# Kernel tuning notes

Measured on AMD Instinct MI355X. Metric: run time of the kernel, lower is better.

Reference implementation:

```python
import jax, jax.numpy as jnp
import numpy as np

V = 20000      # nodes
L = 4          # topological levels
PER = 5000     # nodes per level
DEG = 16       # parents per node
D = 512        # d_model
H = 8          # nheads
Cd = D // H    # head_dim
E = (L - 1) * PER * DEG


def setup_inputs() -> dict:
    rng = np.random.default_rng(0)
    node_levels = np.repeat(np.arange(L), PER).astype(np.int64)
    srcs, tgts = [], []
    for l in range(1, L):
        srcs.append(rng.integers((l - 1) * PER, l * PER, size=PER * DEG))
        tgts.append(np.repeat(np.arange(l * PER, (l + 1) * PER), DEG))
    edge_index = np.stack([np.concatenate(srcs), np.concatenate(tgts)]).astype(np.int64)
    key = jax.random.key(0)
    ks = jax.random.split(key, 14)
    glorot = 0.05
    def p(k, shape):
        return jax.random.normal(k, shape, jnp.float32) * glorot
    return {
        'node_feats': jax.random.normal(ks[0], (V, D), jnp.float32),
        'edge_feats': jax.random.normal(ks[1], (E, D), jnp.float32),
        'edge_index': jnp.asarray(edge_index),
        'node_levels': jnp.asarray(node_levels),
        'n_levels': L,
        'Wn_bu': p(ks[2], (D, D)), 'We_bu': p(ks[3], (D, D)), 'attn_bu': p(ks[4], (H, 3 * Cd)),
        'Wo_bu': p(ks[5], (D, D)), 'bo_bu': jnp.zeros((D,), jnp.float32),
        'Wn_td': p(ks[6], (D, D)), 'We_td': p(ks[7], (D, D)), 'attn_td': p(ks[8], (H, 3 * Cd)),
        'Wo_td': p(ks[9], (D, D)), 'bo_td': jnp.zeros((D,), jnp.float32),
    }


def _direction(node_feats, edge_feats, Wn, We, attn_w, Wo, bo, src, tgt, node_lv, n_levels):
    Vn = node_feats.shape[0]
    scale = (3 * Cd) ** -0.5
    aw_j, aw_i, aw_e = attn_w[:, :Cd], attn_w[:, Cd:2 * Cd], attn_w[:, 2 * Cd:]
    # edge features are static across levels -> project once
    ep = (edge_feats @ We).reshape(-1, H, Cd)            # E h c
    ep_alpha = jnp.einsum('ehc,hc->eh', ep, aw_e)        # E h
    edge_lv = node_lv[tgt]                               # level of each edge's target
    for l in range(1, n_levels):
        xp = (node_feats @ Wn).reshape(Vn, H, Cd)        # V h c
        aj = jnp.einsum('vhc,hc->vh', xp, aw_j)
        ai = jnp.einsum('vhc,hc->vh', xp, aw_i)
        a = (aj[src] + ai[tgt] + ep_alpha) * scale       # E h
        a = jnp.where((edge_lv == l)[:, None], a, -jnp.inf)
        # self-loop: edge feature filled with 0.0 -> only x_j/x_i terms
        sa = (aj + ai) * scale                           # V h
        m = jnp.maximum(jax.ops.segment_max(a, tgt, num_segments=Vn), sa)
        we = jnp.exp(a - m[tgt])                         # E h (0 for masked edges)
        ws = jnp.exp(sa - m)                             # V h
        denom = jax.ops.segment_sum(we, tgt, num_segments=Vn) + ws
        agg = jax.ops.segment_sum(we[:, :, None] * xp[src], tgt, num_segments=Vn) + ws[:, :, None] * xp
        out = (agg / denom[:, :, None]).reshape(Vn, H * Cd) @ Wo + bo  # to_out (dropout=eval identity)
        node_feats = jnp.where((node_lv == l)[:, None], out, node_feats)
    return node_feats


def reference(node_feats, edge_feats, edge_index, node_levels, n_levels,
              Wn_bu, We_bu, attn_bu, Wo_bu, bo_bu,
              Wn_td, We_td, attn_td, Wo_td, bo_td):
    src, tgt = edge_index[0], edge_index[1]
    # bottom-up: edges as given, topo levels 0..L-1
    bu = _direction(node_feats, edge_feats, Wn_bu, We_bu, attn_bu, Wo_bu, bo_bu,
                    src, tgt, node_levels, n_levels)
    # top-down: reversed edges, topo levels reversed
    lv_td = (n_levels - 1) - node_levels
    td = _direction(node_feats, edge_feats, Wn_td, We_td, attn_td, Wo_td, bo_td,
                    tgt, src, lv_td, n_levels)
    return jnp.stack([td, bu], axis=0)  # (topdown, bottomup)
```

## Files before the change

kernel.cpp:

```cpp
#include <hip/hip_runtime.h>

#define NV 20000
#define NE 240000
#define PER 5000
#define DEG 16
#define EPB 80000
#define SCALE 0.07216878364870323f
#define MAXDEG 96

typedef __attribute__((ext_vector_type(8))) short s16x8;
typedef __attribute__((ext_vector_type(4))) float f32x4;

__device__ inline ushort bf16rne(float x) {
    uint32_t u = __float_as_uint(x);
    u += 0x7fffu + ((u >> 16) & 1u);
    return (ushort)(u >> 16);
}
__device__ inline s16x8 cvt8(float4 a, float4 b) {
    s16x8 v;
    v[0] = (short)bf16rne(a.x); v[1] = (short)bf16rne(a.y);
    v[2] = (short)bf16rne(a.z); v[3] = (short)bf16rne(a.w);
    v[4] = (short)bf16rne(b.x); v[5] = (short)bf16rne(b.y);
    v[6] = (short)bf16rne(b.z); v[7] = (short)bf16rne(b.w);
    return v;
}

__global__ void init_copy(const float* __restrict__ nf, float* __restrict__ out) {
    int i = blockIdx.x * 256 + threadIdx.x;
    float4 v = reinterpret_cast<const float4*>(nf)[i];
    reinterpret_cast<float4*>(out)[i] = v;
    reinterpret_cast<float4*>(out + (size_t)NV * 512)[i] = v;
}

__global__ void fold_kernel(
    const float* __restrict__ Wn_bu, const float* __restrict__ attn_bu,
    const float* __restrict__ Wn_td, const float* __restrict__ attn_td,
    const float* __restrict__ We_bu, const float* __restrict__ We_td,
    ushort* __restrict__ foldT)
{
    int idx = blockIdx.x * 256 + threadIdx.x;
    if (idx >= 3 * 8192) return;
    int arr = idx >> 13;
    int r = idx & 8191;
    int d = r >> 4;
    int o = r & 15;
    int h = o & 7;
    const float* W; const float* attn; int awOff;
    if (arr == 0)      { W = Wn_bu; attn = attn_bu; awOff = (o < 8) ? 0 : 64; }
    else if (arr == 1) { W = Wn_td; attn = attn_td; awOff = (o < 8) ? 0 : 64; }
    else               { W = (o < 8) ? We_bu : We_td; attn = (o < 8) ? attn_bu : attn_td; awOff = 128; }
    float s = 0.f;
    for (int cc = 0; cc < 64; ++cc)
        s += W[d * 512 + h * 64 + cc] * attn[h * 192 + awOff + cc];
    foldT[arr * 8192 + o * 512 + d] = bf16rne(s);
}

__global__ __launch_bounds__(256) void prep_w(
    const float* __restrict__ W0, const float* __restrict__ W1,
    const float* __restrict__ W2, const float* __restrict__ W3,
    ushort* __restrict__ Bt)
{
    __shared__ float T[64][65];
    const int t = threadIdx.x;
    const int b = blockIdx.x;
    const int mat = b >> 6;
    const int tk = (b >> 3) & 7, tn = b & 7;
    const float* W = (mat == 0) ? W0 : (mat == 1) ? W1 : (mat == 2) ? W2 : W3;
    const int k0 = tk * 64, n0 = tn * 64;
    #pragma unroll
    for (int i = 0; i < 4; ++i) {
        int r = (t >> 4) * 4 + i;
        int c = (t & 15) * 4;
        float4 v = *reinterpret_cast<const float4*>(W + (size_t)(k0 + r) * 512 + n0 + c);
        T[r][c + 0] = v.x; T[r][c + 1] = v.y; T[r][c + 2] = v.z; T[r][c + 3] = v.w;
    }
    __syncthreads();
    #pragma unroll
    for (int i = 0; i < 4; ++i) {
        int n = (t >> 4) * 4 + i;
        int c = (t & 15) * 4;
        ushort4 o;
        o.x = bf16rne(T[c + 0][n]); o.y = bf16rne(T[c + 1][n]);
        o.z = bf16rne(T[c + 2][n]); o.w = bf16rne(T[c + 3][n]);
        *reinterpret_cast<ushort4*>(Bt + (size_t)mat * 262144 + (size_t)(n0 + n) * 512 + k0 + c) = o;
    }
}

__global__ __launch_bounds__(256) void rowdot_mfma(
    const float* __restrict__ A, int nTiles,
    const ushort* __restrict__ Bt16, float* __restrict__ out)
{
    __shared__ ushort Bs[16][520];
    const int t = threadIdx.x;
    for (int i = t; i < 16 * 512; i += 256)
        Bs[i >> 9][i & 511] = Bt16[i];
    __syncthreads();
    const int wave = t >> 6, lane = t & 63;
    const int tile = blockIdx.x * 4 + wave;
    if (tile >= nTiles) return;
    const int fr = lane & 15;
    const int fk = (lane >> 4) * 8;
    const float* Ar = A + (size_t)tile * 16 * 512 + (size_t)fr * 512;
    f32x4 acc = {0.f, 0.f, 0.f, 0.f};
    #pragma unroll
    for (int k0 = 0; k0 < 512; k0 += 32) {
        float4 a0 = *reinterpret_cast<const float4*>(Ar + k0 + fk);
        float4 a1 = *reinterpret_cast<const float4*>(Ar + k0 + fk + 4);
        s16x8 av = cvt8(a0, a1);
        s16x8 bv = *reinterpret_cast<const s16x8*>(&Bs[fr][k0 + fk]);
        acc = __builtin_amdgcn_mfma_f32_16x16x32_bf16(av, bv, acc, 0, 0, 0);
    }
    #pragma unroll
    for (int i = 0; i < 4; ++i) {
        int r = tile * 16 + (lane >> 4) * 4 + i;
        out[(size_t)r * 16 + (lane & 15)] = acc[i];
    }
}

__global__ __launch_bounds__(256) void gemm_mfma(
    const float* __restrict__ A, const ushort* __restrict__ Bt,
    float* __restrict__ C, int M, const float* __restrict__ bias)
{
    __shared__ ushort As[64][40];
    __shared__ ushort Bs[64][40];
    const int t = threadIdx.x;
    const int wave = t >> 6, lane = t & 63;
    const int row0 = blockIdx.x * 64, col0 = blockIdx.y * 64;
    const int wm = (wave >> 1) * 32, wn = (wave & 1) * 32;
    const int sm = t >> 2;
    const int sk = (t & 3) * 8;
    const int fr = lane & 15;
    const int fk = (lane >> 4) * 8;
    const bool aok = (row0 + sm) < M;
    const float* Ap = A + (size_t)(row0 + sm) * 512;
    const ushort* Bp = Bt + (size_t)(col0 + sm) * 512;
    f32x4 acc[2][2];
    #pragma unroll
    for (int mi = 0; mi < 2; ++mi)
        #pragma unroll
        for (int ni = 0; ni < 2; ++ni) acc[mi][ni] = (f32x4){0.f, 0.f, 0.f, 0.f};

    for (int k0 = 0; k0 < 512; k0 += 32) {
        float4 a0, a1;
        if (aok) {
            a0 = *reinterpret_cast<const float4*>(Ap + k0 + sk);
            a1 = *reinterpret_cast<const float4*>(Ap + k0 + sk + 4);
        } else {
            a0 = make_float4(0.f, 0.f, 0.f, 0.f);
            a1 = a0;
        }
        *reinterpret_cast<s16x8*>(&As[sm][sk]) = cvt8(a0, a1);
        *reinterpret_cast<s16x8*>(&Bs[sm][sk]) =
            *reinterpret_cast<const s16x8*>(Bp + k0 + sk);
        __syncthreads();
        s16x8 af[2], bf[2];
        af[0] = *reinterpret_cast<const s16x8*>(&As[wm + fr][fk]);
        af[1] = *reinterpret_cast<const s16x8*>(&As[wm + 16 + fr][fk]);
        bf[0] = *reinterpret_cast<const s16x8*>(&Bs[wn + fr][fk]);
        bf[1] = *reinterpret_cast<const s16x8*>(&Bs[wn + 16 + fr][fk]);
        acc[0][0] = __builtin_amdgcn_mfma_f32_16x16x32_bf16(af[0], bf[0], acc[0][0], 0, 0, 0);
        acc[0][1] = __builtin_amdgcn_mfma_f32_16x16x32_bf16(af[0], bf[1], acc[0][1], 0, 0, 0);
        acc[1][0] = __builtin_amdgcn_mfma_f32_16x16x32_bf16(af[1], bf[0], acc[1][0], 0, 0, 0);
        acc[1][1] = __builtin_amdgcn_mfma_f32_16x16x32_bf16(af[1], bf[1], acc[1][1], 0, 0, 0);
        __syncthreads();
    }
    #pragma unroll
    for (int mi = 0; mi < 2; ++mi) {
        #pragma unroll
        for (int ni = 0; ni < 2; ++ni) {
            int c = col0 + wn + ni * 16 + (lane & 15);
            float bb = bias ? bias[c] : 0.f;
            #pragma unroll
            for (int i = 0; i < 4; ++i) {
                int r = row0 + wm + mi * 16 + (lane >> 4) * 4 + i;
                if (r < M) C[(size_t)r * 512 + c] = acc[mi][ni][i] + bb;
            }
        }
    }
}

__global__ void csr_zero(int* cnt) {
    int i = blockIdx.x * 256 + threadIdx.x;
    if (i < 15000) cnt[i] = 0;
}
__global__ void csr_count(const int* __restrict__ ei, int* __restrict__ cnt) {
    int e = blockIdx.x * 256 + threadIdx.x;
    if (e >= NE) return;
    int lv = e / EPB;
    int local = ei[e] - lv * PER;
    atomicAdd(&cnt[lv * PER + local], 1);
}
__global__ void csr_scan(const int* __restrict__ cnt, int* __restrict__ rptr) {
    __shared__ int part[256];
    int lv = blockIdx.x, t = threadIdx.x;
    int s = 0;
    if (t < 250)
        for (int j = 0; j < 20; ++j) s += cnt[lv * PER + t * 20 + j];
    part[t] = s;
    __syncthreads();
    if (t == 0) {
        int run = 0;
        for (int i = 0; i < 250; ++i) { int v = part[i]; part[i] = run; run += v; }
        rptr[lv * 5001 + 5000] = run;
    }
    __syncthreads();
    if (t < 250) {
        int run = part[t];
        for (int j = 0; j < 20; ++j) {
            int idx = t * 20 + j;
            rptr[lv * 5001 + idx] = run;
            run += cnt[lv * PER + idx];
        }
    }
}
__global__ void csr_offinit(const int* __restrict__ rptr, int* __restrict__ off) {
    int i = blockIdx.x * 256 + threadIdx.x;
    if (i >= 15000) return;
    int lv = i / PER, local = i - lv * PER;
    off[i] = rptr[lv * 5001 + local];
}
__global__ void csr_fill(const int* __restrict__ ei, int* __restrict__ off, int* __restrict__ eids) {
    int e = blockIdx.x * 256 + threadIdx.x;
    if (e >= NE) return;
    int lv = e / EPB;
    int local = ei[e] - lv * PER;
    int pos = atomicAdd(&off[lv * PER + local], 1);
    eids[lv * EPB + pos] = e;
}

template<bool FIXED>
__global__ __launch_bounds__(512) void attn_kernel(
    const float* __restrict__ xp,
    const float* __restrict__ ajai,
    const float* __restrict__ epA,
    const int* __restrict__ srcArr,
    const int* __restrict__ rptr,
    const int* __restrict__ eids,
    int eBase,
    int base,
    int tgtLocOff,
    int dirOff,
    float* __restrict__ aggn)
{
    __shared__ float Lwe[MAXDEG][8];
    __shared__ int   Lsrci[MAXDEG];
    __shared__ float Lws[8];
    __shared__ float Ldenom[8];
    const int t = blockIdx.x;
    const int tid = threadIdx.x;
    const int tgtXp = tgtLocOff + t;

    int deg, ebase;
    if (FIXED) { deg = DEG; ebase = eBase + t * DEG; }
    else       { int r0 = rptr[t]; deg = rptr[t + 1] - r0; ebase = r0; }
    if (deg > MAXDEG) deg = MAXDEG;

    for (int kk = tid; kk < deg * 8; kk += 512) {
        int k = kk >> 3, h = kk & 7;
        int e = FIXED ? (ebase + k) : eids[ebase + k];
        int src = srcArr[e] - base;
        float lg = (ajai[src * 16 + h] + ajai[tgtXp * 16 + 8 + h] + epA[(size_t)e * 16 + dirOff + h]) * SCALE;
        Lwe[k][h] = lg;
        if (h == 0) Lsrci[k] = src;
    }
    if (tid < 8) Lws[tid] = (ajai[tgtXp * 16 + tid] + ajai[tgtXp * 16 + 8 + tid]) * SCALE;
    __syncthreads();
    if (tid < 8) {
        float m = Lws[tid];
        for (int k = 0; k < deg; ++k) m = fmaxf(m, Lwe[k][tid]);
        float dsum = 0.f;
        for (int k = 0; k < deg; ++k) {
            float w = expf(Lwe[k][tid] - m);
            Lwe[k][tid] = w;
            dsum += w;
        }
        float wsv = expf(Lws[tid] - m);
        Lws[tid] = wsv;
        Ldenom[tid] = dsum + wsv;
    }
    __syncthreads();
    const int h = tid >> 6, c = tid & 63;
    float acc = Lws[h] * xp[(size_t)tgtXp * 512 + h * 64 + c];
    if (FIXED) {
        #pragma unroll
        for (int k = 0; k < DEG; ++k)
            acc += Lwe[k][h] * xp[(size_t)Lsrci[k] * 512 + h * 64 + c];
    } else {
        #pragma unroll 4
        for (int k = 0; k < deg; ++k)
            acc += Lwe[k][h] * xp[(size_t)Lsrci[k] * 512 + h * 64 + c];
    }
    aggn[(size_t)t * 512 + h * 64 + c] = acc / Ldenom[h];
}

extern "C" void kernel_launch(void* const* d_in, const int* in_sizes, int n_in,
                              void* d_out, int out_size, void* d_ws, size_t ws_size,
                              hipStream_t stream) {
    const float* node_feats = (const float*)d_in[0];
    const float* edge_feats = (const float*)d_in[1];
    const int*   edge_index = (const int*)d_in[2];
    const float* Wn_bu  = (const float*)d_in[5];
    const float* We_bu  = (const float*)d_in[6];
    const float* attn_bu = (const float*)d_in[7];
    const float* Wo_bu  = (const float*)d_in[8];
    const float* bo_bu  = (const float*)d_in[9];
    const float* Wn_td  = (const float*)d_in[10];
    const float* We_td  = (const float*)d_in[11];
    const float* attn_td = (const float*)d_in[12];
    const float* Wo_td  = (const float*)d_in[13];
    const float* bo_td  = (const float*)d_in[14];

    float* out = (float*)d_out;
    float* td = out;
    float* bu = out + (size_t)NV * 512;

    float* ws   = (float*)d_ws;
    float* xp   = ws;
    float* aggn = xp + 5120000;
    float* ajai = aggn + 2560000;
    float* epA  = ajai + 160000;
    int* cnt  = (int*)(epA + 3840000);
    int* off  = cnt + 15000;
    int* rptr = off + 15000;
    int* eids = rptr + 15008;
    ushort* BtW   = (ushort*)(eids + 240000);
    ushort* foldT = BtW + 4 * 262144;

    const int* ei_src = edge_index;
    const int* ei_tgt = edge_index + NE;

    init_copy<<<10000, 256, 0, stream>>>(node_feats, out);
    fold_kernel<<<96, 256, 0, stream>>>(Wn_bu, attn_bu, Wn_td, attn_td, We_bu, We_td, foldT);
    prep_w<<<256, 256, 0, stream>>>(Wn_bu, Wo_bu, Wn_td, Wo_td, BtW);
    rowdot_mfma<<<3750, 256, 0, stream>>>(edge_feats, 15000, foldT + 2 * 8192, epA);

    csr_zero<<<59, 256, 0, stream>>>(cnt);
    csr_count<<<938, 256, 0, stream>>>(ei_src, cnt);
    csr_scan<<<3, 256, 0, stream>>>(cnt, rptr);
    csr_offinit<<<59, 256, 0, stream>>>(rptr, off);
    csr_fill<<<938, 256, 0, stream>>>(ei_src, off, eids);

    for (int l = 1; l <= 3; ++l) {
        int base = (l - 1) * PER;
        gemm_mfma<<<dim3(157, 8), 256, 0, stream>>>(bu + (size_t)base * 512, BtW, xp, 10000, nullptr);
        rowdot_mfma<<<157, 256, 0, stream>>>(bu + (size_t)base * 512, 625, foldT, ajai);
        attn_kernel<true><<<5000, 512, 0, stream>>>(xp, ajai, epA, ei_src,
                                                    nullptr, nullptr, (l - 1) * EPB,
                                                    base, PER, 0, aggn);
        gemm_mfma<<<dim3(79, 8), 256, 0, stream>>>(aggn, BtW + 262144, bu + (size_t)(l * PER) * 512, 5000, bo_bu);
    }
    for (int ltd = 1; ltd <= 3; ++ltd) {
        int lvIdx = 3 - ltd;
        int base = lvIdx * PER;
        gemm_mfma<<<dim3(157, 8), 256, 0, stream>>>(td + (size_t)base * 512, BtW + 2 * 262144, xp, 10000, nullptr);
        rowdot_mfma<<<157, 256, 0, stream>>>(td + (size_t)base * 512, 625, foldT + 8192, ajai);
        attn_kernel<false><<<5000, 512, 0, stream>>>(xp, ajai, epA, ei_tgt,
                                                     rptr + lvIdx * 5001, eids + lvIdx * EPB, 0,
                                                     base, 0, 8, aggn);
        gemm_mfma<<<dim3(79, 8), 256, 0, stream>>>(aggn, BtW + 3 * 262144, td + (size_t)base * 512, 5000, bo_td);
    }
}
```

Measured before the change: 1.248 ms.

## Batch bottom-up and top-down directions per level and fold attention dots into GEMM

The bottom-up and top-down passes now run together at each level: each GEMM and the attention kernel cover both directions in one launch, selected by grid z or block index. The attention-logit projections (aj/ai) become extra output columns of the node projection GEMM (Bt padded to 576 columns), which removes the separate rowdot launches. The attention kernel handles four targets per block with float4 loads, and the CSR offset init is merged into the scan. Launch count drops and each grid is larger, at the cost of duplicated workspace buffers and some wasted zero-padded GEMM columns.

```diff
diff --git a/kernel.cpp b/kernel.cpp
--- a/kernel.cpp
+++ b/kernel.cpp
@@ -36,29 +36,47 @@
     const float* __restrict__ Wn_bu, const float* __restrict__ attn_bu,
     const float* __restrict__ Wn_td, const float* __restrict__ attn_td,
     const float* __restrict__ We_bu, const float* __restrict__ We_td,
-    ushort* __restrict__ foldT)
+    ushort* __restrict__ Bt1_bu, ushort* __restrict__ Bt1_td,
+    ushort* __restrict__ foldE)
 {
     int idx = blockIdx.x * 256 + threadIdx.x;
-    if (idx >= 3 * 8192) return;
-    int arr = idx >> 13;
-    int r = idx & 8191;
-    int d = r >> 4;
-    int o = r & 15;
-    int h = o & 7;
-    const float* W; const float* attn; int awOff;
-    if (arr == 0)      { W = Wn_bu; attn = attn_bu; awOff = (o < 8) ? 0 : 64; }
-    else if (arr == 1) { W = Wn_td; attn = attn_td; awOff = (o < 8) ? 0 : 64; }
-    else               { W = (o < 8) ? We_bu : We_td; attn = (o < 8) ? attn_bu : attn_td; awOff = 128; }
-    float s = 0.f;
-    for (int cc = 0; cc < 64; ++cc)
-        s += W[d * 512 + h * 64 + cc] * attn[h * 192 + awOff + cc];
-    foldT[arr * 8192 + o * 512 + d] = bf16rne(s);
+    const int SZ = 64 * 512;
+    if (idx < 2 * SZ) {
+        int arr = idx / SZ;
+        int r = idx - arr * SZ;
+        int o = r >> 9;
+        int d = r & 511;
+        ushort val = 0;
+        if (o < 16) {
+            const float* W    = arr ? Wn_td   : Wn_bu;
+            const float* attn = arr ? attn_td : attn_bu;
+            int h = o & 7;
+            int awOff = (o < 8) ? 0 : 64;
+            float s = 0.f;
+            for (int cc = 0; cc < 64; ++cc)
+                s += W[d * 512 + h * 64 + cc] * attn[h * 192 + awOff + cc];
+            val = bf16rne(s);
+        }
+        (arr ? Bt1_td : Bt1_bu)[(size_t)(512 + o) * 512 + d] = val;
+    } else if (idx < 2 * SZ + 16 * 512) {
+        int r = idx - 2 * SZ;
+        int o = r >> 9;
+        int d = r & 511;
+        const float* W    = (o < 8) ? We_bu   : We_td;
+        const float* attn = (o < 8) ? attn_bu : attn_td;
+        int h = o & 7;
+        float s = 0.f;
+        for (int cc = 0; cc < 64; ++cc)
+            s += W[d * 512 + h * 64 + cc] * attn[h * 192 + 128 + cc];
+        foldE[o * 512 + d] = bf16rne(s);
+    }
 }
 
 __global__ __launch_bounds__(256) void prep_w(
     const float* __restrict__ W0, const float* __restrict__ W1,
     const float* __restrict__ W2, const float* __restrict__ W3,
-    ushort* __restrict__ Bt)
+    ushort* __restrict__ Bt1_bu, ushort* __restrict__ Bt2_bu,
+    ushort* __restrict__ Bt1_td, ushort* __restrict__ Bt2_td)
 {
     __shared__ float T[64][65];
     const int t = threadIdx.x;
@@ -66,6 +84,7 @@
     const int mat = b >> 6;
     const int tk = (b >> 3) & 7, tn = b & 7;
     const float* W = (mat == 0) ? W0 : (mat == 1) ? W1 : (mat == 2) ? W2 : W3;
+    ushort* outp = (mat == 0) ? Bt1_bu : (mat == 1) ? Bt2_bu : (mat == 2) ? Bt1_td : Bt2_td;
     const int k0 = tk * 64, n0 = tn * 64;
     #pragma unroll
     for (int i = 0; i < 4; ++i) {
@@ -82,7 +101,7 @@
         ushort4 o;
         o.x = bf16rne(T[c + 0][n]); o.y = bf16rne(T[c + 1][n]);
         o.z = bf16rne(T[c + 2][n]); o.w = bf16rne(T[c + 3][n]);
-        *reinterpret_cast<ushort4*>(Bt + (size_t)mat * 262144 + (size_t)(n0 + n) * 512 + k0 + c) = o;
+        *reinterpret_cast<ushort4*>(outp + (size_t)(n0 + n) * 512 + k0 + c) = o;
     }
 }
 
@@ -117,12 +136,20 @@
     }
 }
 
-__global__ __launch_bounds__(256) void gemm_mfma(
-    const float* __restrict__ A, const ushort* __restrict__ Bt,
-    float* __restrict__ C, int M, const float* __restrict__ bias)
+__global__ __launch_bounds__(256) void gemm1_fused(
+    const float* __restrict__ Abu, const float* __restrict__ Atd,
+    const ushort* __restrict__ Btbu, const ushort* __restrict__ Bttd,
+    float* __restrict__ xpbu, float* __restrict__ xptd,
+    float* __restrict__ ajbu, float* __restrict__ ajtd)
 {
     __shared__ ushort As[64][40];
     __shared__ ushort Bs[64][40];
+    const int z = blockIdx.z;
+    const float* A   = z ? Atd  : Abu;
+    const ushort* Bt = z ? Bttd : Btbu;
+    float* xp = z ? xptd : xpbu;
+    float* aj = z ? ajtd : ajbu;
+    const int M = 10000;
     const int t = threadIdx.x;
     const int wave = t >> 6, lane = t & 63;
     const int row0 = blockIdx.x * 64, col0 = blockIdx.y * 64;
@@ -169,7 +196,79 @@
         #pragma unroll
         for (int ni = 0; ni < 2; ++ni) {
             int c = col0 + wn + ni * 16 + (lane & 15);
-            float bb = bias ? bias[c] : 0.f;
+            #pragma unroll
+            for (int i = 0; i < 4; ++i) {
+                int r = row0 + wm + mi * 16 + (lane >> 4) * 4 + i;
+                if (r < M) {
+                    if (c < 512)       xp[(size_t)r * 512 + c] = acc[mi][ni][i];
+                    else if (c < 528)  aj[(size_t)r * 16 + (c - 512)] = acc[mi][ni][i];
+                }
+            }
+        }
+    }
+}
+
+__global__ __launch_bounds__(256) void gemm2_fused(
+    const float* __restrict__ Abu, const float* __restrict__ Atd,
+    const ushort* __restrict__ Btbu, const ushort* __restrict__ Bttd,
+    float* __restrict__ Cbu, float* __restrict__ Ctd,
+    const float* __restrict__ bbu, const float* __restrict__ btd)
+{
+    __shared__ ushort As[64][40];
+    __shared__ ushort Bs[64][40];
+    const int z = blockIdx.z;
+    const float* A   = z ? Atd  : Abu;
+    const ushort* Bt = z ? Bttd : Btbu;
+    float* C = z ? Ctd : Cbu;
+    const float* bias = z ? btd : bbu;
+    const int M = 5000;
+    const int t = threadIdx.x;
+    const int wave = t >> 6, lane = t & 63;
+    const int row0 = blockIdx.x * 64, col0 = blockIdx.y * 64;
+    const int wm = (wave >> 1) * 32, wn = (wave & 1) * 32;
+    const int sm = t >> 2;
+    const int sk = (t & 3) * 8;
+    const int fr = lane & 15;
+    const int fk = (lane >> 4) * 8;
+    const bool aok = (row0 + sm) < M;
+    const float* Ap = A + (size_t)(row0 + sm) * 512;
+    const ushort* Bp = Bt + (size_t)(col0 + sm) * 512;
+    f32x4 acc[2][2];
+    #pragma unroll
+    for (int mi = 0; mi < 2; ++mi)
+        #pragma unroll
+        for (int ni = 0; ni < 2; ++ni) acc[mi][ni] = (f32x4){0.f, 0.f, 0.f, 0.f};
+
+    for (int k0 = 0; k0 < 512; k0 += 32) {
+        float4 a0, a1;
+        if (aok) {
+            a0 = *reinterpret_cast<const float4*>(Ap + k0 + sk);
+            a1 = *reinterpret_cast<const float4*>(Ap + k0 + sk + 4);
+        } else {
+            a0 = make_float4(0.f, 0.f, 0.f, 0.f);
+            a1 = a0;
+        }
+        *reinterpret_cast<s16x8*>(&As[sm][sk]) = cvt8(a0, a1);
+        *reinterpret_cast<s16x8*>(&Bs[sm][sk]) =
+            *reinterpret_cast<const s16x8*>(Bp + k0 + sk);
+        __syncthreads();
+        s16x8 af[2], bf[2];
+        af[0] = *reinterpret_cast<const s16x8*>(&As[wm + fr][fk]);
+        af[1] = *reinterpret_cast<const s16x8*>(&As[wm + 16 + fr][fk]);
+        bf[0] = *reinterpret_cast<const s16x8*>(&Bs[wn + fr][fk]);
+        bf[1] = *reinterpret_cast<const s16x8*>(&Bs[wn + 16 + fr][fk]);
+        acc[0][0] = __builtin_amdgcn_mfma_f32_16x16x32_bf16(af[0], bf[0], acc[0][0], 0, 0, 0);
+        acc[0][1] = __builtin_amdgcn_mfma_f32_16x16x32_bf16(af[0], bf[1], acc[0][1], 0, 0, 0);
+        acc[1][0] = __builtin_amdgcn_mfma_f32_16x16x32_bf16(af[1], bf[0], acc[1][0], 0, 0, 0);
+        acc[1][1] = __builtin_amdgcn_mfma_f32_16x16x32_bf16(af[1], bf[1], acc[1][1], 0, 0, 0);
+        __syncthreads();
+    }
+    #pragma unroll
+    for (int mi = 0; mi < 2; ++mi) {
+        #pragma unroll
+        for (int ni = 0; ni < 2; ++ni) {
+            int c = col0 + wn + ni * 16 + (lane & 15);
+            float bb = bias[c];
             #pragma unroll
             for (int i = 0; i < 4; ++i) {
                 int r = row0 + wm + mi * 16 + (lane >> 4) * 4 + i;
@@ -190,7 +289,8 @@
     int local = ei[e] - lv * PER;
     atomicAdd(&cnt[lv * PER + local], 1);
 }
-__global__ void csr_scan(const int* __restrict__ cnt, int* __restrict__ rptr) {
+__global__ void csr_scan(const int* __restrict__ cnt, int* __restrict__ rptr,
+                         int* __restrict__ off) {
     __shared__ int part[256];
     int lv = blockIdx.x, t = threadIdx.x;
     int s = 0;
@@ -209,15 +309,10 @@
         for (int j = 0; j < 20; ++j) {
             int idx = t * 20 + j;
             rptr[lv * 5001 + idx] = run;
+            off[lv * PER + idx] = run;
             run += cnt[lv * PER + idx];
         }
     }
-}
-__global__ void csr_offinit(const int* __restrict__ rptr, int* __restrict__ off) {
-    int i = blockIdx.x * 256 + threadIdx.x;
-    if (i >= 15000) return;
-    int lv = i / PER, local = i - lv * PER;
-    off[i] = rptr[lv * 5001 + local];
 }
 __global__ void csr_fill(const int* __restrict__ ei, int* __restrict__ off, int* __restrict__ eids) {
     int e = blockIdx.x * 256 + threadIdx.x;
@@ -228,69 +323,86 @@
     eids[lv * EPB + pos] = e;
 }
 
-template<bool FIXED>
-__global__ __launch_bounds__(512) void attn_kernel(
-    const float* __restrict__ xp,
-    const float* __restrict__ ajai,
+__global__ __launch_bounds__(512) void attn_fused(
+    const float* __restrict__ xp_bu, const float* __restrict__ ajai_bu,
+    const float* __restrict__ xp_td, const float* __restrict__ ajai_td,
     const float* __restrict__ epA,
-    const int* __restrict__ srcArr,
+    const int* __restrict__ ei_src, const int* __restrict__ ei_tgt,
     const int* __restrict__ rptr,
     const int* __restrict__ eids,
-    int eBase,
-    int base,
-    int tgtLocOff,
-    int dirOff,
-    float* __restrict__ aggn)
-{
-    __shared__ float Lwe[MAXDEG][8];
-    __shared__ int   Lsrci[MAXDEG];
-    __shared__ float Lws[8];
-    __shared__ float Ldenom[8];
-    const int t = blockIdx.x;
+    int eBaseBU, int baseBU, int baseTD,
+    float* __restrict__ aggn_bu, float* __restrict__ aggn_td)
+{
+    __shared__ float Lwe[4][MAXDEG][8];
+    __shared__ int   Lsrci[4][MAXDEG];
+    __shared__ float Lws[4][8];
+    __shared__ float Ldenom[4][8];
     const int tid = threadIdx.x;
-    const int tgtXp = tgtLocOff + t;
+    const int q = tid >> 7, f = tid & 127;
+    const bool isBU = blockIdx.x < 1250;
+    const int t = (isBU ? blockIdx.x : blockIdx.x - 1250) * 4 + q;
+
+    const float* xp   = isBU ? xp_bu   : xp_td;
+    const float* ajai = isBU ? ajai_bu : ajai_td;
+    const int* srcArr = isBU ? ei_src  : ei_tgt;
+    const int base    = isBU ? baseBU  : baseTD;
+    const int tgtXp   = (isBU ? 5000 : 0) + t;
+    const int dirOff  = isBU ? 0 : 8;
+    float* aggn       = isBU ? aggn_bu : aggn_td;
 
     int deg, ebase;
-    if (FIXED) { deg = DEG; ebase = eBase + t * DEG; }
-    else       { int r0 = rptr[t]; deg = rptr[t + 1] - r0; ebase = r0; }
+    if (isBU) { deg = DEG; ebase = eBaseBU + t * DEG; }
+    else      { int r0 = rptr[t]; deg = rptr[t + 1] - r0; ebase = r0; }
     if (deg > MAXDEG) deg = MAXDEG;
 
-    for (int kk = tid; kk < deg * 8; kk += 512) {
+    const float tAi = ajai[tgtXp * 16 + 8 + (f & 7)];
+    for (int kk = f; kk < deg * 8; kk += 128) {
         int k = kk >> 3, h = kk & 7;
-        int e = FIXED ? (ebase + k) : eids[ebase + k];
+        int e = isBU ? (ebase + k) : eids[ebase + k];
         int src = srcArr[e] - base;
-        float lg = (ajai[src * 16 + h] + ajai[tgtXp * 16 + 8 + h] + epA[(size_t)e * 16 + dirOff + h]) * SCALE;
-        Lwe[k][h] = lg;
-        if (h == 0) Lsrci[k] = src;
-    }
-    if (tid < 8) Lws[tid] = (ajai[tgtXp * 16 + tid] + ajai[tgtXp * 16 + 8 + tid]) * SCALE;
-    __syncthreads();
-    if (tid < 8) {
-        float m = Lws[tid];
-        for (int k = 0; k < deg; ++k) m = fmaxf(m, Lwe[k][tid]);
+        float lg = (ajai[src * 16 + h] + tAi + epA[(size_t)e * 16 + dirOff + h]) * SCALE;
+        Lwe[q][k][h] = lg;
+        if (h == 0) Lsrci[q][k] = src;
+    }
+    if (f < 8) Lws[q][f] = (ajai[tgtXp * 16 + f] + ajai[tgtXp * 16 + 8 + f]) * SCALE;
+    __syncthreads();
+    if (f < 8) {
+        float m = Lws[q][f];
+        for (int k = 0; k < deg; ++k) m = fmaxf(m, Lwe[q][k][f]);
         float dsum = 0.f;
         for (int k = 0; k < deg; ++k) {
-            float w = expf(Lwe[k][tid] - m);
-            Lwe[k][tid] = w;
+            float w = expf(Lwe[q][k][f] - m);
+            Lwe[q][k][f] = w;
             dsum += w;
         }
-        float wsv = expf(Lws[tid] - m);
-        Lws[tid] = wsv;
-        Ldenom[tid] = dsum + wsv;
-    }
-    __syncthreads();
-    const int h = tid >> 6, c = tid & 63;
-    float acc = Lws[h] * xp[(size_t)tgtXp * 512 + h * 64 + c];
-    if (FIXED) {
+        float wsv = expf(Lws[q][f] - m);
+        Lws[q][f] = wsv;
+        Ldenom[q][f] = dsum + wsv;
+    }
+    __syncthreads();
+    const int h = f >> 4;
+    const float4* xp4 = reinterpret_cast<const float4*>(xp);
+    float4 xv = xp4[(size_t)tgtXp * 128 + f];
+    float w0 = Lws[q][h];
+    float ax = w0 * xv.x, ay = w0 * xv.y, az = w0 * xv.z, aw = w0 * xv.w;
+    if (isBU) {
         #pragma unroll
-        for (int k = 0; k < DEG; ++k)
-            acc += Lwe[k][h] * xp[(size_t)Lsrci[k] * 512 + h * 64 + c];
+        for (int k = 0; k < DEG; ++k) {
+            float w = Lwe[q][k][h];
+            float4 v = xp4[(size_t)Lsrci[q][k] * 128 + f];
+            ax += w * v.x; ay += w * v.y; az += w * v.z; aw += w * v.w;
+        }
     } else {
         #pragma unroll 4
-        for (int k = 0; k < deg; ++k)
-            acc += Lwe[k][h] * xp[(size_t)Lsrci[k] * 512 + h * 64 + c];
-    }
-    aggn[(size_t)t * 512 + h * 64 + c] = acc / Ldenom[h];
+        for (int k = 0; k < deg; ++k) {
+            float w = Lwe[q][k][h];
+            float4 v = xp4[(size_t)Lsrci[q][k] * 128 + f];
+            ax += w * v.x; ay += w * v.y; az += w * v.z; aw += w * v.w;
+        }
+    }
+    float inv = 1.f / Ldenom[q][h];
+    float4 r; r.x = ax * inv; r.y = ay * inv; r.z = az * inv; r.w = aw * inv;
+    reinterpret_cast<float4*>(aggn)[(size_t)t * 128 + f] = r;
 }
 
 extern "C" void kernel_launch(void* const* d_in, const int* in_sizes, int n_in,
@@ -314,49 +426,53 @@
     float* td = out;
     float* bu = out + (size_t)NV * 512;
 
-    float* ws   = (float*)d_ws;
-    float* xp   = ws;
-    float* aggn = xp + 5120000;
-    float* ajai = aggn + 2560000;
-    float* epA  = ajai + 160000;
+    float* ws      = (float*)d_ws;
+    float* xp_bu   = ws;
+    float* xp_td   = xp_bu + 5120000;
+    float* aggn_bu = xp_td + 5120000;
+    float* aggn_td = aggn_bu + 2560000;
+    float* ajai_bu = aggn_td + 2560000;
+    float* ajai_td = ajai_bu + 160000;
+    float* epA     = ajai_td + 160000;
     int* cnt  = (int*)(epA + 3840000);
     int* off  = cnt + 15000;
     int* rptr = off + 15000;
     int* eids = rptr + 15008;
-    ushort* BtW   = (ushort*)(eids + 240000);
-    ushort* foldT = BtW + 4 * 262144;
+    ushort* Bt1_bu = (ushort*)(eids + 240000);
+    ushort* Bt1_td = Bt1_bu + 294912;
+    ushort* Bt2_bu = Bt1_td + 294912;
+    ushort* Bt2_td = Bt2_bu + 262144;
+    ushort* foldE  = Bt2_td + 262144;
 
     const int* ei_src = edge_index;
     const int* ei_tgt = edge_index + NE;
 
     init_copy<<<10000, 256, 0, stream>>>(node_feats, out);
-    fold_kernel<<<96, 256, 0, stream>>>(Wn_bu, attn_bu, Wn_td, attn_td, We_bu, We_td, foldT);
-    prep_w<<<256, 256, 0, stream>>>(Wn_bu, Wo_bu, Wn_td, Wo_td, BtW);
-    rowdot_mfma<<<3750, 256, 0, stream>>>(edge_feats, 15000, foldT + 2 * 8192, epA);
+    fold_kernel<<<288, 256, 0, stream>>>(Wn_bu, attn_bu, Wn_td, attn_td, We_bu, We_td,
+                                         Bt1_bu, Bt1_td, foldE);
+    prep_w<<<256, 256, 0, stream>>>(Wn_bu, Wo_bu, Wn_td, Wo_td,
+                                    Bt1_bu, Bt2_bu, Bt1_td, Bt2_td);
+    rowdot_mfma<<<3750, 256, 0, stream>>>(edge_feats, 15000, foldE, epA);
 
     csr_zero<<<59, 256, 0, stream>>>(cnt);
     csr_count<<<938, 256, 0, stream>>>(ei_src, cnt);
-    csr_scan<<<3, 256, 0, stream>>>(cnt, rptr);
-    csr_offinit<<<59, 256, 0, stream>>>(rptr, off);
+    csr_scan<<<3, 256, 0, stream>>>(cnt, rptr, off);
     csr_fill<<<938, 256, 0, stream>>>(ei_src, off, eids);
 
-    for (int l = 1; l <= 3; ++l) {
-        int base = (l - 1) * PER;
-        gemm_mfma<<<dim3(157, 8), 256, 0, stream>>>(bu + (size_t)base * 512, BtW, xp, 10000, nullptr);
-        rowdot_mfma<<<157, 256, 0, stream>>>(bu + (size_t)base * 512, 625, foldT, ajai);
-        attn_kernel<true><<<5000, 512, 0, stream>>>(xp, ajai, epA, ei_src,
-                                                    nullptr, nullptr, (l - 1) * EPB,
-                                                    base, PER, 0, aggn);
-        gemm_mfma<<<dim3(79, 8), 256, 0, stream>>>(aggn, BtW + 262144, bu + (size_t)(l * PER) * 512, 5000, bo_bu);
-    }
-    for (int ltd = 1; ltd <= 3; ++ltd) {
-        int lvIdx = 3 - ltd;
-        int base = lvIdx * PER;
-        gemm_mfma<<<dim3(157, 8), 256, 0, stream>>>(td + (size_t)base * 512, BtW + 2 * 262144, xp, 10000, nullptr);
-        rowdot_mfma<<<157, 256, 0, stream>>>(td + (size_t)base * 512, 625, foldT + 8192, ajai);
-        attn_kernel<false><<<5000, 512, 0, stream>>>(xp, ajai, epA, ei_tgt,
-                                                     rptr + lvIdx * 5001, eids + lvIdx * EPB, 0,
-                                                     base, 0, 8, aggn);
-        gemm_mfma<<<dim3(79, 8), 256, 0, stream>>>(aggn, BtW + 3 * 262144, td + (size_t)base * 512, 5000, bo_td);
-    }
-}
+    for (int i = 1; i <= 3; ++i) {
+        const int l = i, lvIdx = 3 - i;
+        const int baseBU = (l - 1) * PER;
+        const int baseTD = lvIdx * PER;
+        gemm1_fused<<<dim3(157, 9, 2), 256, 0, stream>>>(
+            bu + (size_t)baseBU * 512, td + (size_t)baseTD * 512,
+            Bt1_bu, Bt1_td, xp_bu, xp_td, ajai_bu, ajai_td);
+        attn_fused<<<2500, 512, 0, stream>>>(
+            xp_bu, ajai_bu, xp_td, ajai_td, epA, ei_src, ei_tgt,
+            rptr + lvIdx * 5001, eids + (size_t)lvIdx * EPB,
+            (l - 1) * EPB, baseBU, baseTD, aggn_bu, aggn_td);
+        gemm2_fused<<<dim3(79, 8, 2), 256, 0, stream>>>(
+            aggn_bu, aggn_td, Bt2_bu, Bt2_td,
+            bu + (size_t)l * PER * 512, td + (size_t)baseTD * 512,
+            bo_bu, bo_td);
+    }
+}
```

Result: faster. 1.172 ms (-6.0%).
